# Kernel tuning notes

Measured on AMD Instinct MI355X. Metric: run time of the kernel, lower is better.

## Reference

```python
import jax, jax.numpy as jnp
import numpy as np

N_NODES = 200000
N_EDGES = 1600000
NUM_GRAPHS = 2000
VOCAB = 10000
D = 64
NUM_CLS = 2


def setup_inputs() -> dict:
    key = jax.random.key(0)
    ks = jax.random.split(key, 12)
    x = jax.random.randint(ks[0], (N_NODES,), 0, VOCAB, dtype=jnp.int32)
    edge_index = jax.random.randint(ks[1], (2, N_EDGES), 0, N_NODES, dtype=jnp.int32)
    edge_type = jax.random.randint(ks[2], (N_EDGES,), 0, 8, dtype=jnp.int32)
    batch = jnp.sort(jax.random.randint(ks[3], (N_NODES,), 0, NUM_GRAPHS, dtype=jnp.int32))
    embed_table = jax.random.normal(ks[4], (VOCAB, D), dtype=jnp.float32) * 0.02
    embed_table = embed_table.at[0].set(0.0)  # padding_idx=0
    W1 = jax.random.normal(ks[5], (D, D), dtype=jnp.float32) * (1.0 / np.sqrt(D))
    b1 = jnp.zeros((D,), dtype=jnp.float32)
    W2 = jax.random.normal(ks[6], (D, D), dtype=jnp.float32) * (1.0 / np.sqrt(D))
    b2 = jnp.zeros((D,), dtype=jnp.float32)
    Wlin = jax.random.normal(ks[7], (D, NUM_CLS), dtype=jnp.float32) * (1.0 / np.sqrt(D))
    blin = jnp.zeros((NUM_CLS,), dtype=jnp.float32)
    return {"x": x, "edge_index": edge_index, "edge_type": edge_type, "batch": batch,
            "embed_table": embed_table, "W1": W1, "b1": b1, "W2": W2, "b2": b2,
            "Wlin": Wlin, "blin": blin}


def reference(x, edge_index, edge_type, batch, embed_table, W1, b1, W2, b2, Wlin, blin):
    n = x.shape[0]
    # GCN normalization with self-loops (PyG GCNConv default, edge weight = 1)
    loops = jnp.arange(n, dtype=edge_index.dtype)
    src = jnp.concatenate([edge_index[0], loops])
    dst = jnp.concatenate([edge_index[1], loops])
    deg = jax.ops.segment_sum(jnp.ones_like(src, dtype=jnp.float32), dst, num_segments=n)
    dinv = jax.lax.rsqrt(deg)  # deg >= 1 due to self-loops
    norm = (dinv[src] * dinv[dst])[:, None]  # [E+N, 1]

    def gcn(h, W, b):
        h = h @ W  # transform first (small GEMM)
        agg = jax.ops.segment_sum(norm * h[src], dst, num_segments=n)
        return agg + b

    h = embed_table[x]                      # [N, D] embedding lookup
    h = jax.nn.relu(gcn(h, W1, b1))
    h = jax.nn.relu(gcn(h, W2, b2))
    # global mean pool over graphs
    sums = jax.ops.segment_sum(h, batch, num_segments=NUM_GRAPHS)
    cnts = jax.ops.segment_sum(jnp.ones((n,), dtype=h.dtype), batch, num_segments=NUM_GRAPHS)
    g = sums / jnp.maximum(cnts, 1.0)[:, None]
    return g @ Wlin + blin
```

## Files before the change

### kernel.cpp

```cpp
#include <hip/hip_runtime.h>
#include <hip/hip_fp16.h>


#define DD 64
#define BKT 256
#define MAXK 1024
#define NBLK 256
#define SLACK 772
#define BTE 1024
#define SRCMASK 0x3FFFF

typedef _Float16 half8_t __attribute__((ext_vector_type(8)));
typedef float float4_t __attribute__((ext_vector_type(4)));
union F4H8 { float4 f; half8_t h; };
union H8   { float4 f; __half2 h[4]; };

static __device__ __forceinline__ void atomAddF(float* p, float v) {
    unsafeAtomicAdd(p, v);
}

__global__ __launch_bounds__(BTE) void bin_count_kernel(
        const int* __restrict__ dst, int E, int CH,
        int* __restrict__ hist, int K,
        const float2* __restrict__ table2, __half2* __restrict__ th2, int n2,
        const float* __restrict__ W1, const float* __restrict__ W2,
        __half* __restrict__ w1t, __half* __restrict__ w2t) {
    __shared__ int lh[MAXK];
    int tid = threadIdx.x;
    for (int i = tid; i < K; i += BTE) lh[i] = 0;
    __syncthreads();
    int stride = gridDim.x * BTE;
    for (int i = blockIdx.x * BTE + tid; i < n2; i += stride)
        th2[i] = __float22half2_rn(table2[i]);
    for (int i = blockIdx.x * BTE + tid; i < DD * DD; i += stride) {
        int n = i >> 6, k = i & 63;
        w1t[i] = __float2half(W1[k * DD + n]);
        w2t[i] = __float2half(W2[k * DD + n]);
    }
    int e0 = blockIdx.x * CH;
    int e1 = min(E, e0 + CH);
    for (int e = e0 + tid; e < e1; e += BTE)
        atomicAdd(&lh[((unsigned)dst[e]) >> 8], 1);
    __syncthreads();
    for (int b = tid; b < K; b += BTE)
        hist[blockIdx.x * MAXK + b] = lh[b];
}

__global__ __launch_bounds__(256) void totals_kernel(
        const int* __restrict__ hist, int* __restrict__ bts,
        float* __restrict__ outacc, int K, int G2) {
    int gt = blockIdx.x * 256 + threadIdx.x;
    if (gt < G2) outacc[gt] = 0.f;
    int wid = gt >> 6;
    int lane = threadIdx.x & 63;
    if (wid >= K) return;
    const int PER = NBLK / 64;
    int s = 0;
    #pragma unroll
    for (int i = 0; i < PER; ++i)
        s += hist[(lane * PER + i) * MAXK + wid];
    #pragma unroll
    for (int off = 32; off >= 1; off >>= 1)
        s += __shfl_xor(s, off);
    if (lane == 0) bts[wid] = s;
}

__global__ __launch_bounds__(256) void scan_bb_kernel(
        const int* __restrict__ bts, int* __restrict__ bb, int K, int E) {
    __shared__ int part[256];
    int tid = threadIdx.x;
    int CH2 = (K + 255) / 256;
    int base = tid * CH2;
    int s = 0;
    for (int i = 0; i < CH2; ++i) {
        int idx = base + i;
        if (idx < K) s += bts[idx];
    }
    part[tid] = s;
    __syncthreads();
    if (tid < 64) {
        int carry = 0;
        for (int c = 0; c < 4; ++c) {
            int orig = part[c * 64 + tid];
            int v = orig;
            #pragma unroll
            for (int off = 1; off < 64; off <<= 1) {
                int t = __shfl_up(v, off);
                if (tid >= off) v += t;
            }
            int tot = __shfl(v, 63);
            part[c * 64 + tid] = v - orig + carry;
            carry += tot;
        }
    }
    __syncthreads();
    int run = part[tid];
    for (int i = 0; i < CH2; ++i) {
        int idx = base + i;
        if (idx < K) {
            bb[idx] = run;
            run += bts[idx];
        }
    }
    if (tid == 0) bb[K] = E;
}

__global__ __launch_bounds__(256) void scanB_kernel(
        const int* __restrict__ hist, const int* __restrict__ bb,
        int* __restrict__ cur, int K) {
    int wid = (blockIdx.x * 256 + threadIdx.x) >> 6;
    int lane = threadIdx.x & 63;
    if (wid >= K) return;
    int b = wid;
    const int PER = NBLK / 64;
    int v[PER];
    int sum = 0;
    #pragma unroll
    for (int i = 0; i < PER; ++i) {
        v[i] = hist[(lane * PER + i) * MAXK + b];
        sum += v[i];
    }
    int pref = sum;
    #pragma unroll
    for (int off = 1; off < 64; off <<= 1) {
        int t = __shfl_up(pref, off);
        if (lane >= off) pref += t;
    }
    int run = bb[b] + pref - sum;
    #pragma unroll
    for (int i = 0; i < PER; ++i) {
        cur[(lane * PER + i) * MAXK + b] = run;
        run += v[i];
    }
}

__global__ __launch_bounds__(BTE) void fill_kernel(
        const int* __restrict__ src, const int* __restrict__ dst, int E, int CH,
        const int* __restrict__ cur, int* __restrict__ pairbuf, int K) {
    __shared__ int lcur[MAXK];
    int tid = threadIdx.x;
    for (int b = tid; b < K; b += BTE)
        lcur[b] = cur[blockIdx.x * MAXK + b];
    __syncthreads();
    int e0 = blockIdx.x * CH;
    int e1 = min(E, e0 + CH);
    for (int e = e0 + tid; e < e1; e += BTE) {
        int s = src[e], d = dst[e];
        int pos = atomicAdd(&lcur[((unsigned)d) >> 8], 1);
        pairbuf[pos] = s | ((d & 255) << 24);
    }
}

__global__ __launch_bounds__(256) void build_csr_kernel(
        const int* __restrict__ pairbuf, const int* __restrict__ bnd,
        const int* __restrict__ x, int2* __restrict__ rowinfo,
        float2* __restrict__ xd, __half* __restrict__ dinvh,
        int* __restrict__ csr_src, __half* __restrict__ g1h, int N) {
    __shared__ int cnt[256], basel[256], curl[256];
    int tid = threadIdx.x;
    int b = blockIdx.x;
    int node0 = b << 8;
    cnt[tid] = 0;
    __syncthreads();
    int bb0 = bnd[b], bb1 = bnd[b + 1];
    for (int i = bb0 + tid; i < bb1; i += 256)
        atomicAdd(&cnt[((unsigned)pairbuf[i]) >> 24], 1);
    __syncthreads();
    int c  = cnt[tid];
    int pc = (c + 3) & ~3;
    {
        __syncthreads();
        basel[tid] = pc;
        __syncthreads();
        if (tid < 64) {
            int carry = 0;
            for (int cc = 0; cc < 4; ++cc) {
                int orig = basel[cc * 64 + tid];
                int v = orig;
                #pragma unroll
                for (int off = 1; off < 64; off <<= 1) {
                    int t = __shfl_up(v, off);
                    if (tid >= off) v += t;
                }
                int tot = __shfl(v, 63);
                cnt[cc * 64 + tid] = v - orig + carry;
                carry += tot;
            }
        }
        __syncthreads();
    }
    int cb0 = ((bb0 + 3) & ~3) + SLACK * b;
    int node = node0 + tid;
    int myBase = cb0 + cnt[tid];
    curl[tid] = myBase;
    if (node < N) {
        rowinfo[node] = make_int2(myBase, pc);
        float di = rsqrtf((float)c + 1.0f);
        xd[node] = make_float2(di, __int_as_float(x[node]));
        dinvh[node] = __float2half(di);
        for (int t = c; t < pc; ++t) csr_src[myBase + t] = N;
    } else if (node == N) {
        xd[N] = make_float2(0.0f, __int_as_float(0));
        dinvh[N] = __float2half(0.0f);
        float2* z = (float2*)(g1h + (size_t)N * DD);
        for (int t = 0; t < DD / 4; ++t) z[t] = make_float2(0.f, 0.f);
    }
    __syncthreads();
    for (int i = bb0 + tid; i < bb1; i += 256) {
        int pk = pairbuf[i];
        int pos = atomicAdd(&curl[((unsigned)pk) >> 24], 1);
        int s = pk & 0x00FFFFFF;
        csr_src[pos] = (int)(((unsigned)s) | (((unsigned)x[s]) << 18));
    }
}

__global__ __launch_bounds__(256, 8) void layer1_kernel(
        const int2* __restrict__ rowinfo,
        const int* __restrict__ csr_src, const float2* __restrict__ xd,
        const __half* __restrict__ dinvh,
        const float4* __restrict__ th4, const __half* __restrict__ wt,
        const float* __restrict__ bias, __half* __restrict__ g1h, int N) {
    __shared__ float4 Hs4[32 * 9];
    __shared__ float dvs[32];
    int row0 = blockIdx.x * 32;
    int tid = threadIdx.x;
    int node_l = tid >> 3, j3 = tid & 7;
    int node = row0 + node_l;
    H8 acc0, acc1, acc2, acc3;
    acc0.f = make_float4(0.f, 0.f, 0.f, 0.f);
    acc1.f = acc0.f; acc2.f = acc0.f; acc3.f = acc0.f;
    __half2 dh = __float2half2_rn(0.f);
    if (node < N) {
        float2 sxd = xd[node];
        float di = sxd.x;
        if (j3 == 0) dvs[node_l] = di;
        dh = __float2half2_rn(di);
        H8 tv; tv.f = th4[(size_t)__float_as_int(sxd.y) * 8 + j3];
        acc0.h[0] = __hmul2(dh, tv.h[0]); acc0.h[1] = __hmul2(dh, tv.h[1]);
        acc0.h[2] = __hmul2(dh, tv.h[2]); acc0.h[3] = __hmul2(dh, tv.h[3]);
        int2 ri = rowinfo[node];
        const int4* cs = (const int4*)(csr_src + ri.x);
        int nq = ri.y >> 2;
        int q = 0;
        for (; q + 1 < nq; q += 2) {
            int4 sA = cs[q], sB = cs[q + 1];
            unsigned a0 = (unsigned)sA.x, a1 = (unsigned)sA.y;
            unsigned a2 = (unsigned)sA.z, a3 = (unsigned)sA.w;
            unsigned b0i = (unsigned)sB.x, b1i = (unsigned)sB.y;
            unsigned b2i = (unsigned)sB.z, b3i = (unsigned)sB.w;
            H8 u0, u1, u2, u3, u4, u5, u6, u7;
            u0.f = th4[(size_t)(a0 >> 18) * 8 + j3];
            u1.f = th4[(size_t)(a1 >> 18) * 8 + j3];
            u2.f = th4[(size_t)(a2 >> 18) * 8 + j3];
            u3.f = th4[(size_t)(a3 >> 18) * 8 + j3];
            u4.f = th4[(size_t)(b0i >> 18) * 8 + j3];
            u5.f = th4[(size_t)(b1i >> 18) * 8 + j3];
            u6.f = th4[(size_t)(b2i >> 18) * 8 + j3];
            u7.f = th4[(size_t)(b3i >> 18) * 8 + j3];
            __half2 w0 = __half2half2(dinvh[a0 & SRCMASK]);
            __half2 w1 = __half2half2(dinvh[a1 & SRCMASK]);
            __half2 w2 = __half2half2(dinvh[a2 & SRCMASK]);
            __half2 w3 = __half2half2(dinvh[a3 & SRCMASK]);
            __half2 w4 = __half2half2(dinvh[b0i & SRCMASK]);
            __half2 w5 = __half2half2(dinvh[b1i & SRCMASK]);
            __half2 w6 = __half2half2(dinvh[b2i & SRCMASK]);
            __half2 w7 = __half2half2(dinvh[b3i & SRCMASK]);
            #pragma unroll
            for (int t = 0; t < 4; ++t) {
                acc0.h[t] = __hfma2(w0, u0.h[t], acc0.h[t]);
                acc1.h[t] = __hfma2(w1, u1.h[t], acc1.h[t]);
                acc2.h[t] = __hfma2(w2, u2.h[t], acc2.h[t]);
                acc3.h[t] = __hfma2(w3, u3.h[t], acc3.h[t]);
                acc0.h[t] = __hfma2(w4, u4.h[t], acc0.h[t]);
                acc1.h[t] = __hfma2(w5, u5.h[t], acc1.h[t]);
                acc2.h[t] = __hfma2(w6, u6.h[t], acc2.h[t]);
                acc3.h[t] = __hfma2(w7, u7.h[t], acc3.h[t]);
            }
        }
        if (q < nq) {
            int4 sA = cs[q];
            unsigned a0 = (unsigned)sA.x, a1 = (unsigned)sA.y;
            unsigned a2 = (unsigned)sA.z, a3 = (unsigned)sA.w;
            H8 u0, u1, u2, u3;
            u0.f = th4[(size_t)(a0 >> 18) * 8 + j3];
            u1.f = th4[(size_t)(a1 >> 18) * 8 + j3];
            u2.f = th4[(size_t)(a2 >> 18) * 8 + j3];
            u3.f = th4[(size_t)(a3 >> 18) * 8 + j3];
            __half2 w0 = __half2half2(dinvh[a0 & SRCMASK]);
            __half2 w1 = __half2half2(dinvh[a1 & SRCMASK]);
            __half2 w2 = __half2half2(dinvh[a2 & SRCMASK]);
            __half2 w3 = __half2half2(dinvh[a3 & SRCMASK]);
            #pragma unroll
            for (int t = 0; t < 4; ++t) {
                acc0.h[t] = __hfma2(w0, u0.h[t], acc0.h[t]);
                acc1.h[t] = __hfma2(w1, u1.h[t], acc1.h[t]);
                acc2.h[t] = __hfma2(w2, u2.h[t], acc2.h[t]);
                acc3.h[t] = __hfma2(w3, u3.h[t], acc3.h[t]);
            }
        }
        #pragma unroll
        for (int t = 0; t < 4; ++t)
            acc0.h[t] = __hmul2(dh, __hadd2(__hadd2(acc0.h[t], acc1.h[t]),
                                            __hadd2(acc2.h[t], acc3.h[t])));
    }
    Hs4[node_l * 9 + j3] = acc0.f;
    __syncthreads();

    int wave = tid >> 6, lane = tid & 63;
    int m = lane & 15, quad = lane >> 4;
    int ncol = wave * 16 + m;
    F4H8 b0, b1;
    const float4* WT4 = (const float4*)wt;
    b0.f = WT4[ncol * 8 + quad];
    b1.f = WT4[ncol * 8 + 4 + quad];
    float bb_ = bias[ncol];
    #pragma unroll
    for (int t = 0; t < 2; ++t) {
        F4H8 a0, a1;
        a0.f = Hs4[(t * 16 + m) * 9 + quad];
        a1.f = Hs4[(t * 16 + m) * 9 + 4 + quad];
        float4_t acc = {0.f, 0.f, 0.f, 0.f};
        acc = __builtin_amdgcn_mfma_f32_16x16x32_f16(a0.h, b0.h, acc, 0, 0, 0);
        acc = __builtin_amdgcn_mfma_f32_16x16x32_f16(a1.h, b1.h, acc, 0, 0, 0);
        #pragma unroll
        for (int reg = 0; reg < 4; ++reg) {
            int row = t * 16 + quad * 4 + reg;
            int grow = row0 + row;
            if (grow < N) {
                float h = fmaxf(acc[reg] + bb_, 0.0f);
                g1h[(size_t)grow * DD + ncol] = __float2half(dvs[row] * h);
            }
        }
    }
}

__global__ __launch_bounds__(256, 8) void layer2_pool_kernel(
        const int2* __restrict__ rowinfo,
        const int* __restrict__ csr_src, const float2* __restrict__ xd,
        const float4* __restrict__ g1h4, const __half* __restrict__ wt,
        const float* __restrict__ bias, const int* __restrict__ batch,
        const float* __restrict__ Wlin, float* __restrict__ outacc, int N) {
    __shared__ float4 Hs4[32 * 9];
    __shared__ float lp0[128], lp1[128];
    __shared__ float p0s[32], p1s[32];
    __shared__ int   bat[32];
    int row0 = blockIdx.x * 32;
    int tid = threadIdx.x;
    int node_l = tid >> 3, j3 = tid & 7;
    int node = row0 + node_l;
    H8 acc0, acc1, acc2, acc3;
    acc0.f = make_float4(0.f, 0.f, 0.f, 0.f);
    acc1.f = acc0.f; acc2.f = acc0.f; acc3.f = acc0.f;
    if (node < N) {
        float di = xd[node].x;
        acc0.f = g1h4[(size_t)node * 8 + j3];
        int2 ri = rowinfo[node];
        const int4* cs = (const int4*)(csr_src + ri.x);
        int nq = ri.y >> 2;
        int q = 0;
        for (; q + 1 < nq; q += 2) {
            int4 sA = cs[q], sB = cs[q + 1];
            H8 u0, u1, u2, u3, u4, u5, u6, u7;
            u0.f = g1h4[(size_t)(sA.x & SRCMASK) * 8 + j3];
            u1.f = g1h4[(size_t)(sA.y & SRCMASK) * 8 + j3];
            u2.f = g1h4[(size_t)(sA.z & SRCMASK) * 8 + j3];
            u3.f = g1h4[(size_t)(sA.w & SRCMASK) * 8 + j3];
            u4.f = g1h4[(size_t)(sB.x & SRCMASK) * 8 + j3];
            u5.f = g1h4[(size_t)(sB.y & SRCMASK) * 8 + j3];
            u6.f = g1h4[(size_t)(sB.z & SRCMASK) * 8 + j3];
            u7.f = g1h4[(size_t)(sB.w & SRCMASK) * 8 + j3];
            #pragma unroll
            for (int t = 0; t < 4; ++t) {
                acc0.h[t] = __hadd2(acc0.h[t], u0.h[t]);
                acc1.h[t] = __hadd2(acc1.h[t], u1.h[t]);
                acc2.h[t] = __hadd2(acc2.h[t], u2.h[t]);
                acc3.h[t] = __hadd2(acc3.h[t], u3.h[t]);
                acc0.h[t] = __hadd2(acc0.h[t], u4.h[t]);
                acc1.h[t] = __hadd2(acc1.h[t], u5.h[t]);
                acc2.h[t] = __hadd2(acc2.h[t], u6.h[t]);
                acc3.h[t] = __hadd2(acc3.h[t], u7.h[t]);
            }
        }
        if (q < nq) {
            int4 sA = cs[q];
            H8 u0, u1, u2, u3;
            u0.f = g1h4[(size_t)(sA.x & SRCMASK) * 8 + j3];
            u1.f = g1h4[(size_t)(sA.y & SRCMASK) * 8 + j3];
            u2.f = g1h4[(size_t)(sA.z & SRCMASK) * 8 + j3];
            u3.f = g1h4[(size_t)(sA.w & SRCMASK) * 8 + j3];
            #pragma unroll
            for (int t = 0; t < 4; ++t) {
                acc0.h[t] = __hadd2(acc0.h[t], u0.h[t]);
                acc1.h[t] = __hadd2(acc1.h[t], u1.h[t]);
                acc2.h[t] = __hadd2(acc2.h[t], u2.h[t]);
                acc3.h[t] = __hadd2(acc3.h[t], u3.h[t]);
            }
        }
        __half2 dih = __float2half2_rn(di);
        #pragma unroll
        for (int t = 0; t < 4; ++t)
            acc0.h[t] = __hmul2(dih, __hadd2(__hadd2(acc0.h[t], acc1.h[t]),
                                             __hadd2(acc2.h[t], acc3.h[t])));
    }
    Hs4[node_l * 9 + j3] = acc0.f;
    __syncthreads();

    int wave = tid >> 6, lane = tid & 63;
    int m = lane & 15, quad = lane >> 4;
    int ncol = wave * 16 + m;
    F4H8 b0, b1;
    const float4* WT4 = (const float4*)wt;
    b0.f = WT4[ncol * 8 + quad];
    b1.f = WT4[ncol * 8 + 4 + quad];
    float bb_  = bias[ncol];
    float wl0 = Wlin[ncol * 2 + 0];
    float wl1 = Wlin[ncol * 2 + 1];
    #pragma unroll
    for (int t = 0; t < 2; ++t) {
        F4H8 a0, a1;
        a0.f = Hs4[(t * 16 + m) * 9 + quad];
        a1.f = Hs4[(t * 16 + m) * 9 + 4 + quad];
        float4_t acc = {0.f, 0.f, 0.f, 0.f};
        acc = __builtin_amdgcn_mfma_f32_16x16x32_f16(a0.h, b0.h, acc, 0, 0, 0);
        acc = __builtin_amdgcn_mfma_f32_16x16x32_f16(a1.h, b1.h, acc, 0, 0, 0);
        #pragma unroll
        for (int reg = 0; reg < 4; ++reg) {
            int row = t * 16 + quad * 4 + reg;
            int grow = row0 + row;
            float h = (grow < N) ? fmaxf(acc[reg] + bb_, 0.0f) : 0.0f;
            float p0 = h * wl0;
            float p1 = h * wl1;
            #pragma unroll
            for (int off = 8; off >= 1; off >>= 1) {
                p0 += __shfl_xor(p0, off);
                p1 += __shfl_xor(p1, off);
            }
            if (m == 0) {
                lp0[wave * 32 + row] = p0;
                lp1[wave * 32 + row] = p1;
            }
        }
    }
    __syncthreads();
    if (tid < 32) {
        int grow = row0 + tid;
        p0s[tid] = lp0[tid] + lp0[32 + tid] + lp0[64 + tid] + lp0[96 + tid];
        p1s[tid] = lp1[tid] + lp1[32 + tid] + lp1[64 + tid] + lp1[96 + tid];
        bat[tid] = (grow < N) ? batch[grow] : -1;
    }
    __syncthreads();
    if (tid < 32) {
        int bg = bat[tid];
        bool head = (bg >= 0) && (tid == 0 || bat[tid - 1] != bg);
        if (head) {
            float s0 = 0.f, s1 = 0.f;
            for (int k = tid; k < 32 && bat[k] == bg; ++k) {
                s0 += p0s[k];
                s1 += p1s[k];
            }
            atomAddF(&outacc[bg * 2 + 0], s0);
            atomAddF(&outacc[bg * 2 + 1], s1);
        }
    }
}

__global__ void final_kernel(const float* __restrict__ outacc,
                             const int* __restrict__ batch,
                             const float* __restrict__ blin,
                             float* __restrict__ out, int G, int N) {
    int t = blockIdx.x * blockDim.x + threadIdx.x;
    if (t >= G * 2) return;
    int g = t >> 1, c = t & 1;
    int lo = 0, hi = N;
    while (lo < hi) { int m = (lo + hi) >> 1; if (batch[m] < g) lo = m + 1; else hi = m; }
    int lo2 = lo, hi2 = N;
    while (lo2 < hi2) { int m = (lo2 + hi2) >> 1; if (batch[m] < g + 1) lo2 = m + 1; else hi2 = m; }
    float cnt = (float)(lo2 - lo);
    out[t] = outacc[t] / fmaxf(cnt, 1.0f) + blin[c];
}

extern "C" void kernel_launch(void* const* d_in, const int* in_sizes, int n_in,
                              void* d_out, int out_size, void* d_ws, size_t ws_size,
                              hipStream_t stream) {
    const int*   x      = (const int*)d_in[0];
    const int*   ei     = (const int*)d_in[1];
    const int*   batch  = (const int*)d_in[3];
    const float* table  = (const float*)d_in[4];
    const float* W1     = (const float*)d_in[5];
    const float* b1     = (const float*)d_in[6];
    const float* W2     = (const float*)d_in[7];
    const float* b2     = (const float*)d_in[8];
    const float* Wlin   = (const float*)d_in[9];
    const float* blin   = (const float*)d_in[10];
    float* out = (float*)d_out;

    const int N = in_sizes[0];
    const int E = in_sizes[2];
    const int G = out_size / 2;
    const int TBL = in_sizes[4];

    const int* src = ei;
    const int* dst = ei + E;

    const int K = (N + BKT - 1) / BKT;
    const int M = NBLK * MAXK;
    const int CH = (E + NBLK - 1) / NBLK;
    const int CSRSZ = E + SLACK * K + 64;

    __half* g1h     = (__half*)d_ws;
    __half* th      = g1h + (size_t)(N + 1) * DD;
    __half* w1t     = th + TBL;
    __half* w2t     = w1t + DD * DD;
    int*    pairbuf = (int*)(w2t + DD * DD);
    int*    csr_src = pairbuf + E;
    int2*   rowinfo = (int2*)(csr_src + CSRSZ);
    float2* xd      = (float2*)(rowinfo + N);
    __half* dinvh   = (__half*)(xd + N + 1);
    float*  outacc  = (float*)(dinvh + (size_t)((N + 2) & ~1));
    int*    bb      = (int*)(outacc + 2 * G);
    int*    bts     = bb + K + 1;
    int*    hist    = bts + K;
    int*    cur     = hist + M;

    const int BT = 256;

    bin_count_kernel<<<NBLK, BTE, 0, stream>>>(dst, E, CH, hist, K,
                                               (const float2*)table,
                                               (__half2*)th, TBL / 2,
                                               W1, W2, w1t, w2t);
    totals_kernel<<<(K * 64 + BT - 1) / BT, BT, 0, stream>>>(hist, bts, outacc,
                                                             K, 2 * G);
    scan_bb_kernel<<<1, BT, 0, stream>>>(bts, bb, K, E);
    scanB_kernel<<<(K * 64 + BT - 1) / BT, BT, 0, stream>>>(hist, bb, cur, K);
    fill_kernel<<<NBLK, BTE, 0, stream>>>(src, dst, E, CH, cur, pairbuf, K);
    build_csr_kernel<<<K, BT, 0, stream>>>(pairbuf, bb, x, rowinfo, xd, dinvh,
                                           csr_src, g1h, N);

    int gRow = (N + 31) / 32;
    layer1_kernel<<<gRow, BT, 0, stream>>>(rowinfo, csr_src, xd, dinvh,
                                           (const float4*)th, w1t, b1, g1h, N);
    layer2_pool_kernel<<<gRow, BT, 0, stream>>>(rowinfo, csr_src, xd,
                                                (const float4*)g1h, w2t, b2,
                                                batch, Wlin, outacc, N);
    final_kernel<<<(G * 2 + BT - 1) / BT, BT, 0, stream>>>(outacc, batch, blin,
                                                           out, G, N);
}
```

Baseline: 219.6 us.

## Replace two-level bucketed CSR build with per-node global atomic counting sort

Swaps the bucketed histogram/scan/fill/build pipeline for a direct per-node degree count using global atomics, a block-sum plus scan to get row bases, and a placement pass that atomically claims slots per destination node. This removes the intermediate pairbuf pass, the large per-block histogram arrays and the shared-memory bucket sort. In exchange it relies on scattered global atomics on 200k counters and random writes into the CSR array, which may contend or lose locality. Edge order within a row also becomes nondeterministic.

Measured after the change: 362.8 us. 65.2% more time.

```diff
diff --git a/kernel.cpp b/kernel.cpp
--- a/kernel.cpp
+++ b/kernel.cpp
@@ -3,11 +3,6 @@
 
 
 #define DD 64
-#define BKT 256
-#define MAXK 1024
-#define NBLK 256
-#define SLACK 772
-#define BTE 1024
 #define SRCMASK 0x3FFFF
 
 typedef _Float16 half8_t __attribute__((ext_vector_type(8)));
@@ -19,54 +14,48 @@
     unsafeAtomicAdd(p, v);
 }
 
-__global__ __launch_bounds__(BTE) void bin_count_kernel(
-        const int* __restrict__ dst, int E, int CH,
-        int* __restrict__ hist, int K,
+__global__ __launch_bounds__(256) void zero_kernel(
+        int* __restrict__ deg, float* __restrict__ outacc, int N, int G2) {
+    int i = blockIdx.x * 256 + threadIdx.x;
+    if (i < N) deg[i] = 0;
+    if (i < G2) outacc[i] = 0.f;
+}
+
+__global__ __launch_bounds__(256) void count_kernel(
+        const int* __restrict__ dst, int E, int* __restrict__ deg,
         const float2* __restrict__ table2, __half2* __restrict__ th2, int n2,
         const float* __restrict__ W1, const float* __restrict__ W2,
         __half* __restrict__ w1t, __half* __restrict__ w2t) {
-    __shared__ int lh[MAXK];
-    int tid = threadIdx.x;
-    for (int i = tid; i < K; i += BTE) lh[i] = 0;
-    __syncthreads();
-    int stride = gridDim.x * BTE;
-    for (int i = blockIdx.x * BTE + tid; i < n2; i += stride)
+    int i0 = blockIdx.x * 256 + threadIdx.x;
+    int stride = gridDim.x * 256;
+    for (int i = i0; i < n2; i += stride)
         th2[i] = __float22half2_rn(table2[i]);
-    for (int i = blockIdx.x * BTE + tid; i < DD * DD; i += stride) {
+    for (int i = i0; i < DD * DD; i += stride) {
         int n = i >> 6, k = i & 63;
         w1t[i] = __float2half(W1[k * DD + n]);
         w2t[i] = __float2half(W2[k * DD + n]);
     }
-    int e0 = blockIdx.x * CH;
-    int e1 = min(E, e0 + CH);
-    for (int e = e0 + tid; e < e1; e += BTE)
-        atomicAdd(&lh[((unsigned)dst[e]) >> 8], 1);
-    __syncthreads();
-    for (int b = tid; b < K; b += BTE)
-        hist[blockIdx.x * MAXK + b] = lh[b];
-}
-
-__global__ __launch_bounds__(256) void totals_kernel(
-        const int* __restrict__ hist, int* __restrict__ bts,
-        float* __restrict__ outacc, int K, int G2) {
-    int gt = blockIdx.x * 256 + threadIdx.x;
-    if (gt < G2) outacc[gt] = 0.f;
-    int wid = gt >> 6;
-    int lane = threadIdx.x & 63;
-    if (wid >= K) return;
-    const int PER = NBLK / 64;
-    int s = 0;
-    #pragma unroll
-    for (int i = 0; i < PER; ++i)
-        s += hist[(lane * PER + i) * MAXK + wid];
+    for (int e = i0; e < E; e += stride)
+        atomicAdd(&deg[dst[e]], 1);
+}
+
+__global__ __launch_bounds__(256) void blocksum_kernel(
+        const int* __restrict__ deg, int* __restrict__ bsum, int N) {
+    __shared__ int wsum[4];
+    int tid = threadIdx.x;
+    int node = blockIdx.x * 256 + tid;
+    int c = (node < N) ? deg[node] : 0;
+    int pc = (c + 3) & ~3;
     #pragma unroll
     for (int off = 32; off >= 1; off >>= 1)
-        s += __shfl_xor(s, off);
-    if (lane == 0) bts[wid] = s;
-}
-
-__global__ __launch_bounds__(256) void scan_bb_kernel(
-        const int* __restrict__ bts, int* __restrict__ bb, int K, int E) {
+        pc += __shfl_xor(pc, off);
+    if ((tid & 63) == 0) wsum[tid >> 6] = pc;
+    __syncthreads();
+    if (tid == 0) bsum[blockIdx.x] = wsum[0] + wsum[1] + wsum[2] + wsum[3];
+}
+
+__global__ __launch_bounds__(256) void scan_kernel(
+        const int* __restrict__ bsum, int* __restrict__ bbase, int K) {
     __shared__ int part[256];
     int tid = threadIdx.x;
     int CH2 = (K + 255) / 256;
@@ -74,7 +63,7 @@
     int s = 0;
     for (int i = 0; i < CH2; ++i) {
         int idx = base + i;
-        if (idx < K) s += bts[idx];
+        if (idx < K) s += bsum[idx];
     }
     part[tid] = s;
     __syncthreads();
@@ -98,119 +87,68 @@
     for (int i = 0; i < CH2; ++i) {
         int idx = base + i;
         if (idx < K) {
-            bb[idx] = run;
-            run += bts[idx];
-        }
-    }
-    if (tid == 0) bb[K] = E;
-}
-
-__global__ __launch_bounds__(256) void scanB_kernel(
-        const int* __restrict__ hist, const int* __restrict__ bb,
-        int* __restrict__ cur, int K) {
-    int wid = (blockIdx.x * 256 + threadIdx.x) >> 6;
-    int lane = threadIdx.x & 63;
-    if (wid >= K) return;
-    int b = wid;
-    const int PER = NBLK / 64;
-    int v[PER];
-    int sum = 0;
-    #pragma unroll
-    for (int i = 0; i < PER; ++i) {
-        v[i] = hist[(lane * PER + i) * MAXK + b];
-        sum += v[i];
-    }
-    int pref = sum;
-    #pragma unroll
-    for (int off = 1; off < 64; off <<= 1) {
-        int t = __shfl_up(pref, off);
-        if (lane >= off) pref += t;
-    }
-    int run = bb[b] + pref - sum;
-    #pragma unroll
-    for (int i = 0; i < PER; ++i) {
-        cur[(lane * PER + i) * MAXK + b] = run;
-        run += v[i];
-    }
-}
-
-__global__ __launch_bounds__(BTE) void fill_kernel(
-        const int* __restrict__ src, const int* __restrict__ dst, int E, int CH,
-        const int* __restrict__ cur, int* __restrict__ pairbuf, int K) {
-    __shared__ int lcur[MAXK];
-    int tid = threadIdx.x;
-    for (int b = tid; b < K; b += BTE)
-        lcur[b] = cur[blockIdx.x * MAXK + b];
-    __syncthreads();
-    int e0 = blockIdx.x * CH;
-    int e1 = min(E, e0 + CH);
-    for (int e = e0 + tid; e < e1; e += BTE) {
-        int s = src[e], d = dst[e];
-        int pos = atomicAdd(&lcur[((unsigned)d) >> 8], 1);
-        pairbuf[pos] = s | ((d & 255) << 24);
-    }
-}
-
-__global__ __launch_bounds__(256) void build_csr_kernel(
-        const int* __restrict__ pairbuf, const int* __restrict__ bnd,
+            bbase[idx] = run;
+            run += bsum[idx];
+        }
+    }
+}
+
+__global__ __launch_bounds__(256) void rowbase_kernel(
+        const int* __restrict__ deg, const int* __restrict__ bbase,
         const int* __restrict__ x, int2* __restrict__ rowinfo,
         float2* __restrict__ xd, __half* __restrict__ dinvh,
-        int* __restrict__ csr_src, __half* __restrict__ g1h, int N) {
-    __shared__ int cnt[256], basel[256], curl[256];
+        int* __restrict__ cursor, int* __restrict__ csr,
+        __half* __restrict__ g1h, int N) {
+    __shared__ int basel[256], excl[256];
     int tid = threadIdx.x;
-    int b = blockIdx.x;
-    int node0 = b << 8;
-    cnt[tid] = 0;
-    __syncthreads();
-    int bb0 = bnd[b], bb1 = bnd[b + 1];
-    for (int i = bb0 + tid; i < bb1; i += 256)
-        atomicAdd(&cnt[((unsigned)pairbuf[i]) >> 24], 1);
-    __syncthreads();
-    int c  = cnt[tid];
+    int node = blockIdx.x * 256 + tid;
+    int c = (node < N) ? deg[node] : 0;
     int pc = (c + 3) & ~3;
-    {
-        __syncthreads();
-        basel[tid] = pc;
-        __syncthreads();
-        if (tid < 64) {
-            int carry = 0;
-            for (int cc = 0; cc < 4; ++cc) {
-                int orig = basel[cc * 64 + tid];
-                int v = orig;
-                #pragma unroll
-                for (int off = 1; off < 64; off <<= 1) {
-                    int t = __shfl_up(v, off);
-                    if (tid >= off) v += t;
-                }
-                int tot = __shfl(v, 63);
-                cnt[cc * 64 + tid] = v - orig + carry;
-                carry += tot;
-            }
-        }
-        __syncthreads();
-    }
-    int cb0 = ((bb0 + 3) & ~3) + SLACK * b;
-    int node = node0 + tid;
-    int myBase = cb0 + cnt[tid];
-    curl[tid] = myBase;
+    basel[tid] = pc;
+    __syncthreads();
+    if (tid < 64) {
+        int carry = 0;
+        for (int cc = 0; cc < 4; ++cc) {
+            int orig = basel[cc * 64 + tid];
+            int v = orig;
+            #pragma unroll
+            for (int off = 1; off < 64; off <<= 1) {
+                int t = __shfl_up(v, off);
+                if (tid >= off) v += t;
+            }
+            int tot = __shfl(v, 63);
+            excl[cc * 64 + tid] = v - orig + carry;
+            carry += tot;
+        }
+    }
+    __syncthreads();
+    int base = bbase[blockIdx.x] + excl[tid];
     if (node < N) {
-        rowinfo[node] = make_int2(myBase, pc);
+        rowinfo[node] = make_int2(base, pc);
         float di = rsqrtf((float)c + 1.0f);
         xd[node] = make_float2(di, __int_as_float(x[node]));
         dinvh[node] = __float2half(di);
-        for (int t = c; t < pc; ++t) csr_src[myBase + t] = N;
+        cursor[node] = base;
+        for (int t = c; t < pc; ++t) csr[base + t] = N;
     } else if (node == N) {
         xd[N] = make_float2(0.0f, __int_as_float(0));
         dinvh[N] = __float2half(0.0f);
         float2* z = (float2*)(g1h + (size_t)N * DD);
         for (int t = 0; t < DD / 4; ++t) z[t] = make_float2(0.f, 0.f);
     }
-    __syncthreads();
-    for (int i = bb0 + tid; i < bb1; i += 256) {
-        int pk = pairbuf[i];
-        int pos = atomicAdd(&curl[((unsigned)pk) >> 24], 1);
-        int s = pk & 0x00FFFFFF;
-        csr_src[pos] = (int)(((unsigned)s) | (((unsigned)x[s]) << 18));
+}
+
+__global__ __launch_bounds__(256) void place_kernel(
+        const int* __restrict__ src, const int* __restrict__ dstp, int E,
+        const int* __restrict__ x, int* __restrict__ cursor,
+        int* __restrict__ csr) {
+    int i0 = blockIdx.x * 256 + threadIdx.x;
+    int stride = gridDim.x * 256;
+    for (int e = i0; e < E; e += stride) {
+        int s = src[e], d = dstp[e];
+        int xs = x[s];
+        int pos = atomicAdd(&cursor[d], 1);
+        csr[pos] = s | (xs << 18);
     }
 }
 
@@ -502,39 +440,37 @@
     const int* src = ei;
     const int* dst = ei + E;
 
-    const int K = (N + BKT - 1) / BKT;
-    const int M = NBLK * MAXK;
-    const int CH = (E + NBLK - 1) / NBLK;
-    const int CSRSZ = E + SLACK * K + 64;
+    const int KB = (N + 255) / 256;
+    const int CSRSZ = ((E + 3 * N + 64) + 1) & ~1;
 
     __half* g1h     = (__half*)d_ws;
     __half* th      = g1h + (size_t)(N + 1) * DD;
     __half* w1t     = th + TBL;
     __half* w2t     = w1t + DD * DD;
-    int*    pairbuf = (int*)(w2t + DD * DD);
-    int*    csr_src = pairbuf + E;
+    int*    csr_src = (int*)(w2t + DD * DD);
     int2*   rowinfo = (int2*)(csr_src + CSRSZ);
     float2* xd      = (float2*)(rowinfo + N);
     __half* dinvh   = (__half*)(xd + N + 1);
-    float*  outacc  = (float*)(dinvh + (size_t)((N + 2) & ~1));
-    int*    bb      = (int*)(outacc + 2 * G);
-    int*    bts     = bb + K + 1;
-    int*    hist    = bts + K;
-    int*    cur     = hist + M;
+    int*    deg     = (int*)(dinvh + (size_t)((N + 2) & ~1));
+    int*    cursor  = deg + N;
+    int*    bsum    = cursor + N;
+    int*    bbase   = bsum + KB + 1;
+    float*  outacc  = (float*)(bbase + KB + 1);
 
     const int BT = 256;
-
-    bin_count_kernel<<<NBLK, BTE, 0, stream>>>(dst, E, CH, hist, K,
-                                               (const float2*)table,
-                                               (__half2*)th, TBL / 2,
-                                               W1, W2, w1t, w2t);
-    totals_kernel<<<(K * 64 + BT - 1) / BT, BT, 0, stream>>>(hist, bts, outacc,
-                                                             K, 2 * G);
-    scan_bb_kernel<<<1, BT, 0, stream>>>(bts, bb, K, E);
-    scanB_kernel<<<(K * 64 + BT - 1) / BT, BT, 0, stream>>>(hist, bb, cur, K);
-    fill_kernel<<<NBLK, BTE, 0, stream>>>(src, dst, E, CH, cur, pairbuf, K);
-    build_csr_kernel<<<K, BT, 0, stream>>>(pairbuf, bb, x, rowinfo, xd, dinvh,
-                                           csr_src, g1h, N);
+    const int GSTRIDE = 2048;
+
+    int zb = (max(N, 2 * G) + BT - 1) / BT;
+    zero_kernel<<<zb, BT, 0, stream>>>(deg, outacc, N, 2 * G);
+    count_kernel<<<GSTRIDE, BT, 0, stream>>>(dst, E, deg,
+                                             (const float2*)table,
+                                             (__half2*)th, TBL / 2,
+                                             W1, W2, w1t, w2t);
+    blocksum_kernel<<<KB, BT, 0, stream>>>(deg, bsum, N);
+    scan_kernel<<<1, BT, 0, stream>>>(bsum, bbase, KB);
+    rowbase_kernel<<<KB, BT, 0, stream>>>(deg, bbase, x, rowinfo, xd, dinvh,
+                                          cursor, csr_src, g1h, N);
+    place_kernel<<<GSTRIDE, BT, 0, stream>>>(src, dst, E, x, cursor, csr_src);
 
     int gRow = (N + 31) / 32;
     layer1_kernel<<<gRow, BT, 0, stream>>>(rowinfo, csr_src, xd, dinvh,
```
